# Kernel tuning notes

Measured on AMD Instinct MI355X. Metric: run time of the kernel, lower is better.

Reference implementation:

```python
import jax, jax.numpy as jnp
import numpy as np

SEQ, NV, NH, NR = 32768, 256, 512, 256


def _bern(key, p):
    # torch.bernoulli: sample is non-differentiable
    return (jax.random.uniform(key, p.shape, dtype=p.dtype) < p).astype(p.dtype)


def setup_inputs() -> dict:
    key = jax.random.key(0)
    ks = jax.random.split(key, 8)
    f32 = jnp.float32
    return {
        "v_seq": (jax.random.uniform(ks[0], (SEQ, NV), dtype=f32) < 0.1).astype(f32),
        "W1": jax.random.normal(ks[1], (NV, NH), dtype=f32) * 0.01,
        "bv": jnp.zeros((NV,), f32),
        "bh1": jnp.zeros((NH,), f32),
        "W2": jax.random.normal(ks[2], (NH, NH), dtype=f32) * 0.01,
        "bh2": jnp.zeros((NH,), f32),
        "Wyv": jax.random.normal(ks[3], (NV, NR), dtype=f32) * 1e-4,
        "Wyh1": jax.random.normal(ks[4], (NH, NR), dtype=f32) * 1e-4,
        "Wyh2": jax.random.normal(ks[5], (NH, NR), dtype=f32) * 1e-4,
        "Wvu": jax.random.normal(ks[6], (NV, NR), dtype=f32) * 0.01,
        "Wuu": jax.random.normal(ks[7], (NR, NR), dtype=f32) * 0.01,
        "bu": jnp.zeros((NR,), f32),
        "k": 5,
    }


def reference(v_seq, W1, bv, bh1, W2, bh2, Wyv, Wyh1, Wyh2, Wvu, Wuu, bu, k):
    dtype = v_seq.dtype
    nr = Wuu.shape[0]
    seq_len = v_seq.shape[0]

    # vanilla tanh RNN (abstract _run_rnn in base class)
    def rnn_step(u, v):
        u_new = jnp.tanh(v @ Wvu + u @ Wuu + bu)
        return u_new, u_new

    _, rnn_out = jax.lax.scan(rnn_step, jnp.zeros((nr,), dtype), v_seq)
    shifted = jnp.concatenate([jnp.zeros((1, nr), dtype), rnn_out[:-1]], axis=0)

    bv_t = bv + shifted @ Wyv.T    # [S, NV]
    bh1_t = bh1 + shifted @ Wyh1.T  # [S, NH]
    bh2_t = bh2 + shifted @ Wyh2.T  # [S, NH]

    key = jax.random.key(42)

    # CD-k Gibbs chain, RBM1 (visible <-> hidden1)
    v_sample = v_seq
    mean_v = None
    for _ in range(k):
        key, k1, k2 = jax.random.split(key, 3)
        h = _bern(k1, jax.nn.sigmoid(v_sample @ W1 + bh1_t))
        mean_v = jax.nn.sigmoid(h @ W1.T + bv_t)
        v_sample = _bern(k2, mean_v)

    def free_energy1(v):
        return -(v * bv_t).sum(-1) - jax.nn.softplus(v @ W1 + bh1_t).sum(-1)

    cost1 = (free_energy1(v_seq) - free_energy1(jax.lax.stop_gradient(v_sample))).mean()

    # CD-k Gibbs chain, RBM2 (hidden1 <-> hidden2)
    h1 = jax.nn.sigmoid(v_seq @ W1 + bh1_t)
    h1_sample = h1
    for _ in range(k):
        key, k1, k2 = jax.random.split(key, 3)
        h2 = _bern(k1, jax.nn.sigmoid(h1_sample @ W2 + bh2_t))
        h1_sample = _bern(k2, jax.nn.sigmoid(h2 @ W2.T + bh1_t))

    def free_energy2(h):
        return -(h * bh1_t).sum(-1) - jax.nn.softplus(h @ W2 + bh2_t).sum(-1)

    cost2 = (free_energy2(h1) - free_energy2(jax.lax.stop_gradient(h1_sample))).mean()

    eps = 1e-10
    monitor = (v_seq * jnp.log(mean_v + eps)
               + (1.0 - v_seq) * jnp.log(1.0 - mean_v + eps)).sum() / seq_len
    return (cost1 + cost2, monitor)
```

## Files before the change

### kernel.cpp

```cpp
#include <hip/hip_runtime.h>
#include <cstdint>

#define S_LEN 32768
#define NV 256
#define NH 512
#define NR 256

typedef short bf16x8 __attribute__((ext_vector_type(8)));
typedef float f32x4 __attribute__((ext_vector_type(4)));
typedef unsigned short ushort_t;
typedef ushort_t u16x8 __attribute__((ext_vector_type(8)));

__device__ __forceinline__ float b2f(ushort_t u) {
  return __uint_as_float(((uint32_t)u) << 16);
}
__device__ __forceinline__ ushort_t f2b(float f) {
  uint32_t x = __float_as_uint(f);
  uint32_t r = (x + 0x7fffu + ((x >> 16) & 1u)) >> 16;
  return (ushort_t)r;
}

#define TFR(x0,x1,r) { x0 += x1; x1 = ((x1 << (r)) | (x1 >> (32 - (r)))); x1 ^= x0; }
__host__ __forceinline__ void tf2x32(uint32_t k0, uint32_t k1,
                                     uint32_t x0, uint32_t x1,
                                     uint32_t* o0, uint32_t* o1) {
  uint32_t k2 = k0 ^ k1 ^ 0x1BD11BDAu;
  x0 += k0; x1 += k1;
  TFR(x0,x1,13) TFR(x0,x1,15) TFR(x0,x1,26) TFR(x0,x1,6)
  x0 += k1; x1 += k2 + 1u;
  TFR(x0,x1,17) TFR(x0,x1,29) TFR(x0,x1,16) TFR(x0,x1,24)
  x0 += k2; x1 += k0 + 2u;
  TFR(x0,x1,13) TFR(x0,x1,15) TFR(x0,x1,26) TFR(x0,x1,6)
  x0 += k0; x1 += k1 + 3u;
  TFR(x0,x1,17) TFR(x0,x1,29) TFR(x0,x1,16) TFR(x0,x1,24)
  x0 += k1; x1 += k2 + 4u;
  TFR(x0,x1,13) TFR(x0,x1,15) TFR(x0,x1,26) TFR(x0,x1,6)
  x0 += k2; x1 += k0 + 5u;
  *o0 = x0; *o1 = x1;
}

__device__ __forceinline__ float fast_uniform(uint32_t k0, uint32_t k1, uint32_t idx) {
  uint32_t h = idx ^ k0;
  h *= 0xCC9E2D51u; h = (h << 15) | (h >> 17); h *= 0x1B873593u;
  h ^= k1;
  h ^= h >> 16; h *= 0x85EBCA6Bu;
  h ^= h >> 13; h *= 0xC2B2AE35u;
  h ^= h >> 16;
  return __uint_as_float((h >> 9) | 0x3f800000u) - 1.0f;
}

__device__ __forceinline__ float wave_reduce(float v) {
#pragma unroll
  for (int o = 32; o > 0; o >>= 1) v += __shfl_down(v, o, 64);
  return v;
}
__device__ __forceinline__ float softplusf(float z) {
  return fmaxf(z, 0.f) + log1pf(expf(-fabsf(z)));
}

#define F_SAMP  4
#define F_H1    8
#define F_FE    16
#define F_MON   32
#define F_DOTB  64
#define F_DOTS  128

struct GemmArgs {
  const ushort_t* A;
  const ushort_t* BT;
  int boff;
  ushort_t* C;
  ushort_t* C2;
  const float* vseqf;
  double* fe_acc;
  double* mon_acc;
  float sign;
  uint32_t rk0, rk1;
  int N, K, nbx;
};

template<int FLAGS>
__device__ __forceinline__ void run_gemm(const GemmArgs& g,
                                         const ushort_t* __restrict__ biasm, int ldb,
                                         ushort_t* __restrict__ Als,
                                         ushort_t* __restrict__ Bls) {
  const int tid = threadIdx.x;
  const int lane = tid & 63, wave = tid >> 6;
  const int wm = wave >> 1, wn = wave & 1;
  const int q = lane >> 4, l16 = lane & 15;
  const int m0 = blockIdx.y * 128, n0 = blockIdx.x * 128;
  const int N = g.N, K = g.K;

  f32x4 acc[4][4];
#pragma unroll
  for (int mt = 0; mt < 4; mt++)
#pragma unroll
    for (int nt = 0; nt < 4; nt++) {
      const int gn = n0 + wn * 64 + nt * 16 + l16;
      const int gmb = m0 + wm * 64 + mt * 16 + q * 4;
#pragma unroll
      for (int rg = 0; rg < 4; rg++)
        acc[mt][nt][rg] = b2f(biasm[(size_t)(gmb + rg) * ldb + g.boff + gn]);
    }

  for (int kk = 0; kk < K; kk += 64) {
#pragma unroll
    for (int j = 0; j < 4; j++) {
      int c = j * 256 + tid;
      int r = c >> 3, bl = c & 7, bg = bl ^ (r & 7);
      *(uint4*)&Als[r * 64 + bl * 8] =
          *(const uint4*)&g.A[(size_t)(m0 + r) * K + kk + bg * 8];
      *(uint4*)&Bls[r * 64 + bl * 8] =
          *(const uint4*)&g.BT[(size_t)(n0 + r) * K + kk + bg * 8];
    }
    __syncthreads();
#pragma unroll
    for (int c = 0; c < 2; c++) {
      bf16x8 af[4], bf[4];
#pragma unroll
      for (int mt = 0; mt < 4; mt++) {
        int r = wm * 64 + mt * 16 + l16;
        af[mt] = *(const bf16x8*)&Als[r * 64 + (((c * 4 + q) ^ (r & 7)) * 8)];
      }
#pragma unroll
      for (int nt = 0; nt < 4; nt++) {
        int r = wn * 64 + nt * 16 + l16;
        bf[nt] = *(const bf16x8*)&Bls[r * 64 + (((c * 4 + q) ^ (r & 7)) * 8)];
      }
#pragma unroll
      for (int mt = 0; mt < 4; mt++)
#pragma unroll
        for (int nt = 0; nt < 4; nt++)
          acc[mt][nt] = __builtin_amdgcn_mfma_f32_16x16x32_bf16(
              af[mt], bf[nt], acc[mt][nt], 0, 0, 0);
    }
    __syncthreads();
  }

  float fe_sum = 0.f, mon_sum = 0.f;
#pragma unroll
  for (int mt = 0; mt < 4; mt++) {
#pragma unroll
    for (int nt = 0; nt < 4; nt++) {
      const int gn = n0 + wn * 64 + nt * 16 + l16;
      const int gmb = m0 + wm * 64 + mt * 16 + q * 4;
#pragma unroll
      for (int rg = 0; rg < 4; rg++) {
        const int gm = gmb + rg;
        const size_t idx = (size_t)gm * N + gn;
        float z = acc[mt][nt][rg];
        float be = 0.f;
        if constexpr (FLAGS & (F_DOTB | F_DOTS))
          be = b2f(biasm[(size_t)gm * ldb + g.boff + gn]);
        if constexpr (FLAGS & (F_SAMP | F_H1 | F_MON)) {
          float e = __expf(-z);
          if constexpr (FLAGS & F_SAMP) {
            float uu = fast_uniform(g.rk0, g.rk1, (uint32_t)idx);
            bool sbit = fmaf(uu, e, uu) < 1.f;
            g.C[idx] = sbit ? (ushort_t)0x3f80 : (ushort_t)0;
            if constexpr (FLAGS & F_DOTS) fe_sum += sbit ? be : 0.f;
          }
          if constexpr (FLAGS & (F_H1 | F_MON)) {
            float pp = __builtin_amdgcn_rcpf(1.f + e);
            if constexpr (FLAGS & F_H1) g.C2[idx] = f2b(pp);
            if constexpr (FLAGS & F_DOTB) fe_sum += pp * be;
            if constexpr (FLAGS & F_MON) {
              float v = g.vseqf[idx];
              mon_sum += (v != 0.f) ? logf(pp + 1e-10f) : logf(1.f - pp + 1e-10f);
            }
          }
        }
        if constexpr (FLAGS & F_FE) fe_sum += softplusf(z);
      }
    }
  }
  if constexpr (FLAGS & (F_FE | F_DOTB | F_DOTS)) {
    float s = wave_reduce(fe_sum);
    if (lane == 0) atomicAdd(g.fe_acc, (double)(-g.sign * s));
  }
  if constexpr (FLAGS & F_MON) {
    float s = wave_reduce(mon_sum);
    if (lane == 0) atomicAdd(g.mon_acc, (double)s);
  }
}

template<int FLAGS>
__global__ __launch_bounds__(256)
void gemm_samp(GemmArgs g, const ushort_t* __restrict__ biasm, int ldb) {
  __shared__ ushort_t Als[128 * 64];
  __shared__ ushort_t Bls[128 * 64];
  if ((int)blockIdx.x >= g.nbx) return;
  run_gemm<FLAGS>(g, biasm, ldb, Als, Bls);
}

template<int F0, int F1>
__global__ __launch_bounds__(256)
void gemm_pair(GemmArgs g0, GemmArgs g1, const ushort_t* __restrict__ biasm, int ldb) {
  __shared__ ushort_t Als[128 * 64];
  __shared__ ushort_t Bls[128 * 64];
  if (blockIdx.z == 0) {
    if ((int)blockIdx.x >= g0.nbx) return;
    run_gemm<F0>(g0, biasm, ldb, Als, Bls);
  } else {
    if ((int)blockIdx.x >= g1.nbx) return;
    run_gemm<F1>(g1, biasm, ldb, Als, Bls);
  }
}

template<bool OUTF32, bool VDOT>
__global__ __launch_bounds__(256)
void gemm_bias(const ushort_t* __restrict__ A, const ushort_t* __restrict__ BT,
               const float* __restrict__ biasv, ushort_t* __restrict__ Cb,
               float* __restrict__ Cf, const float* __restrict__ vdata,
               double* __restrict__ dacc, int M, int N, int K) {
  __shared__ ushort_t Als[128 * 64];
  __shared__ ushort_t Bls[128 * 64];
  const int tid = threadIdx.x;
  const int lane = tid & 63, wave = tid >> 6;
  const int wm = wave >> 1, wn = wave & 1;
  const int q = lane >> 4, l16 = lane & 15;
  const int m0 = blockIdx.y * 128, n0 = blockIdx.x * 128;

  f32x4 acc[4][4];
#pragma unroll
  for (int i = 0; i < 4; i++)
#pragma unroll
    for (int j = 0; j < 4; j++) acc[i][j] = (f32x4){0.f, 0.f, 0.f, 0.f};

  for (int kk = 0; kk < K; kk += 64) {
#pragma unroll
    for (int j = 0; j < 4; j++) {
      int c = j * 256 + tid;
      int r = c >> 3, bl = c & 7, bg = bl ^ (r & 7);
      *(uint4*)&Als[r * 64 + bl * 8] =
          *(const uint4*)&A[(size_t)(m0 + r) * K + kk + bg * 8];
      *(uint4*)&Bls[r * 64 + bl * 8] =
          *(const uint4*)&BT[(size_t)(n0 + r) * K + kk + bg * 8];
    }
    __syncthreads();
#pragma unroll
    for (int c = 0; c < 2; c++) {
      bf16x8 af[4], bf[4];
#pragma unroll
      for (int mt = 0; mt < 4; mt++) {
        int r = wm * 64 + mt * 16 + l16;
        af[mt] = *(const bf16x8*)&Als[r * 64 + (((c * 4 + q) ^ (r & 7)) * 8)];
      }
#pragma unroll
      for (int nt = 0; nt < 4; nt++) {
        int r = wn * 64 + nt * 16 + l16;
        bf[nt] = *(const bf16x8*)&Bls[r * 64 + (((c * 4 + q) ^ (r & 7)) * 8)];
      }
#pragma unroll
      for (int mt = 0; mt < 4; mt++)
#pragma unroll
        for (int nt = 0; nt < 4; nt++)
          acc[mt][nt] = __builtin_amdgcn_mfma_f32_16x16x32_bf16(
              af[mt], bf[nt], acc[mt][nt], 0, 0, 0);
    }
    __syncthreads();
  }
  float dsum = 0.f;
#pragma unroll
  for (int mt = 0; mt < 4; mt++)
#pragma unroll
    for (int nt = 0; nt < 4; nt++) {
      const int gn = n0 + wn * 64 + nt * 16 + l16;
      const int gmb = m0 + wm * 64 + mt * 16 + q * 4;
      const float bvv = biasv[gn];
#pragma unroll
      for (int rg = 0; rg < 4; rg++) {
        const size_t idx = (size_t)(gmb + rg) * N + gn;
        float z = acc[mt][nt][rg] + bvv;
        if constexpr (OUTF32) Cf[idx] = z; else Cb[idx] = f2b(z);
        if constexpr (VDOT)
          if (n0 < 256) dsum += z * vdata[(size_t)(gmb + rg) * 256 + gn];
      }
    }
  if constexpr (VDOT) {
    if (n0 < 256) {
      float s = wave_reduce(dsum);
      if ((tid & 63) == 0) atomicAdd(dacc, (double)(-s));
    }
  }
}

__global__ __launch_bounds__(1024, 1)
void rnn_scan(const float* __restrict__ Apre, const float* __restrict__ Wuu,
              ushort_t* __restrict__ shifted) {
  const int tid = threadIdx.x;
  const int j = tid >> 2;
  const int s = tid & 3;
  const int t_begin = blockIdx.x * 128;
  const int t_end = t_begin + 128;
  const int t0 = (t_begin >= 16) ? (t_begin - 16) : 0;

  float w[64];
#pragma unroll
  for (int i = 0; i < 64; i++) w[i] = Wuu[(size_t)(s * 64 + i) * 256 + j];

  __shared__ float u[2][280];
  __shared__ float asg[32 * 256];
  if (tid < 256) u[0][(tid >> 6) * 68 + (tid & 63)] = 0.f;
  if (blockIdx.x == 0 && s == 0) shifted[j] = 0;
  __syncthreads();

  const int jp = (j >> 6) * 68 + (j & 63);
  int p = 0;
  for (int tb = t0; tb < t_end; tb += 32) {
    int srow = tb + (tid >> 5);
    if (srow >= S_LEN) srow = S_LEN - 1;
    int scol = (tid & 31) * 8;
    float4 a0 = *(const float4*)&Apre[(size_t)srow * 256 + scol];
    float4 a1 = *(const float4*)&Apre[(size_t)srow * 256 + scol + 4];
    *(float4*)&asg[(tid >> 5) * 256 + scol] = a0;
    *(float4*)&asg[(tid >> 5) * 256 + scol + 4] = a1;
    __syncthreads();
#pragma unroll 1
    for (int i = 0; i < 32; i++) {
      const int t = tb + i;
      if (t >= t_end) break;
      float p0 = 0.f, p1 = 0.f, p2 = 0.f, p3 = 0.f;
#pragma unroll
      for (int qq = 0; qq < 64; qq += 4) {
        float4 uv = *(const float4*)&u[p][s * 68 + qq];
        p0 = fmaf(uv.x, w[qq + 0], p0);
        p1 = fmaf(uv.y, w[qq + 1], p1);
        p2 = fmaf(uv.z, w[qq + 2], p2);
        p3 = fmaf(uv.w, w[qq + 3], p3);
      }
      float ps = (p0 + p1) + (p2 + p3);
      ps += __shfl_xor(ps, 1, 64);
      ps += __shfl_xor(ps, 2, 64);
      float z = asg[i * 256 + j] + ps;
      float e = __expf(2.f * z);
      float unew = 1.f - 2.f * __builtin_amdgcn_rcpf(e + 1.f);
      if (s == 0) {
        u[1 - p][jp] = unew;
        if (t >= t_begin && (t + 1) < S_LEN)
          shifted[(size_t)(t + 1) * 256 + j] = f2b(unew);
      }
      __syncthreads();
      p ^= 1;
    }
  }
}

__global__ __launch_bounds__(256)
void prep_all(const float* __restrict__ v_seq, ushort_t* __restrict__ vseq_bf,
              const float* __restrict__ Wyv, const float* __restrict__ Wyh1,
              const float* __restrict__ Wyh2, ushort_t* __restrict__ Wycat,
              const float* __restrict__ W1, ushort_t* __restrict__ BTw1t,
              ushort_t* __restrict__ BTw1,
              const float* __restrict__ W2, ushort_t* __restrict__ BTw2t,
              ushort_t* __restrict__ BTw2,
              const float* __restrict__ Wvu, ushort_t* __restrict__ BTwvu,
              const float* __restrict__ bv, const float* __restrict__ bh1,
              const float* __restrict__ bh2, float* __restrict__ bveccat) {
  int b = blockIdx.x;
  const int tid = threadIdx.x;
  if (b < 32768) { int i = b * 256 + tid; vseq_bf[i] = f2b(v_seq[i]); return; }
  b -= 32768;
  if (b < 256)  { int i = b * 256 + tid; Wycat[i] = f2b(Wyv[i]); return; }
  b -= 256;
  if (b < 512)  { int i = b * 256 + tid; Wycat[65536 + i] = f2b(Wyh1[i]); return; }
  b -= 512;
  if (b < 512)  { int i = b * 256 + tid; Wycat[196608 + i] = f2b(Wyh2[i]); return; }
  b -= 512;
  if (b < 512)  { int i = b * 256 + tid; BTw1t[i] = f2b(W1[i]); return; }
  b -= 512;
  if (b < 1024) { int i = b * 256 + tid; BTw2t[i] = f2b(W2[i]); return; }
  b -= 1024;
  if (b < 256)  { int i = b * 256 + tid; int r = i >> 8, c = i & 255;
                  BTwvu[c * 256 + r] = f2b(Wvu[i]); return; }
  b -= 256;
  if (b < 512)  { int i = b * 256 + tid; int r = i >> 9, c = i & 511;
                  BTw1[(size_t)c * 256 + r] = f2b(W1[i]); return; }
  b -= 512;
  if (b < 1024) { int i = b * 256 + tid; int r = i >> 9, c = i & 511;
                  BTw2[(size_t)c * 512 + r] = f2b(W2[i]); return; }
  b -= 1024;
  { int i = b * 256 + tid;
    if (i < 1280)
      bveccat[i] = (i < 256) ? bv[i] : (i < 768) ? bh1[i - 256] : bh2[i - 768]; }
}

__global__ void finalize_kernel(const double* __restrict__ acc, float* __restrict__ out) {
  out[0] = (float)(acc[0] / (double)S_LEN);
  out[1] = (float)(acc[1] / (double)S_LEN);
}

extern "C" void kernel_launch(void* const* d_in, const int* in_sizes, int n_in,
                              void* d_out, int out_size, void* d_ws, size_t ws_size,
                              hipStream_t stream) {
  (void)in_sizes; (void)n_in; (void)out_size; (void)ws_size;
  const float* v_seq = (const float*)d_in[0];
  const float* W1    = (const float*)d_in[1];
  const float* bv    = (const float*)d_in[2];
  const float* bh1   = (const float*)d_in[3];
  const float* W2    = (const float*)d_in[4];
  const float* bh2   = (const float*)d_in[5];
  const float* Wyv   = (const float*)d_in[6];
  const float* Wyh1  = (const float*)d_in[7];
  const float* Wyh2  = (const float*)d_in[8];
  const float* Wvu   = (const float*)d_in[9];
  const float* Wuu   = (const float*)d_in[10];
  const float* bu    = (const float*)d_in[11];
  float* out = (float*)d_out;

  const size_t SN = (size_t)S_LEN * NV;
  const size_t SH = (size_t)S_LEN * NH;
  const int NB = NV + NH + NH;
  char* base = (char*)d_ws;
  size_t cur = 0;
  auto take = [&](size_t bytes) { size_t o = cur; cur += (bytes + 255) & ~(size_t)255; return o; };
  double*   acc      = (double*)  (base + take(64));
  ushort_t* BTwvu    = (ushort_t*)(base + take(65536 * 2));
  ushort_t* Wycat    = (ushort_t*)(base + take((size_t)NB * NR * 2));
  float*    bveccat  = (float*)   (base + take(NB * 4));
  ushort_t* BTw1     = (ushort_t*)(base + take(131072 * 2));
  ushort_t* BTw1t    = (ushort_t*)(base + take(131072 * 2));
  ushort_t* BTw2     = (ushort_t*)(base + take(262144 * 2));
  ushort_t* BTw2t    = (ushort_t*)(base + take(262144 * 2));
  ushort_t* vseq_bf  = (ushort_t*)(base + take(SN * 2));
  ushort_t* shifted  = (ushort_t*)(base + take(SN * 2));
  ushort_t* bias_cat = (ushort_t*)(base + take((size_t)S_LEN * NB * 2));
  ushort_t* h1buf    = (ushort_t*)(base + take(SH * 2));
  ushort_t* sampA    = (ushort_t*)(base + take(SH * 2));
  ushort_t* sampB    = (ushort_t*)(base + take(SN * 2));
  float*    Arnn  = (float*)bias_cat;
  ushort_t* sampC = vseq_bf;
  ushort_t* sampD = h1buf;

  uint32_t ka[20], kb[20];
  uint32_t K0 = 0u, K1 = 42u;
  for (int it = 0; it < 10; it++) {
    uint32_t n0, n1, a0, a1, b0, b1;
    tf2x32(K0, K1, 0u, 0u, &n0, &n1);
    tf2x32(K0, K1, 0u, 1u, &a0, &a1);
    tf2x32(K0, K1, 0u, 2u, &b0, &b1);
    ka[2 * it] = a0; kb[2 * it] = a1;
    ka[2 * it + 1] = b0; kb[2 * it + 1] = b1;
    K0 = n0; K1 = n1;
  }

  hipMemsetAsync(acc, 0, 2 * sizeof(double), stream);

  dim3 blk(256);
  prep_all<<<dim3(37381), blk, 0, stream>>>(
      v_seq, vseq_bf, Wyv, Wyh1, Wyh2, Wycat, W1, BTw1t, BTw1,
      W2, BTw2t, BTw2, Wvu, BTwvu, bv, bh1, bh2, bveccat);

  const int M = S_LEN;
  gemm_bias<true, false><<<dim3(2, M / 128), blk, 0, stream>>>(
      vseq_bf, BTwvu, bu, nullptr, Arnn, nullptr, nullptr, M, NV, NV);
  rnn_scan<<<dim3(S_LEN / 128), dim3(1024), 0, stream>>>(Arnn, Wuu, shifted);
  gemm_bias<false, true><<<dim3(NB / 128, M / 128), blk, 0, stream>>>(
      shifted, Wycat, bveccat, bias_cat, nullptr, v_seq, acc, M, NB, NR);

  const int OFF_BV = 0, OFF_BH1 = NV, OFF_BH2 = NV + NH;
  auto mk = [&](const ushort_t* A, const ushort_t* BT, int boff, ushort_t* C,
                ushort_t* C2, const float* vs, float sign, int key, int N, int K) {
    GemmArgs g;
    g.A = A; g.BT = BT; g.boff = boff; g.C = C; g.C2 = C2; g.vseqf = vs;
    g.fe_acc = acc; g.mon_acc = acc + 1; g.sign = sign;
    g.rk0 = key >= 0 ? ka[key] : 0; g.rk1 = key >= 0 ? kb[key] : 0;
    g.N = N; g.K = K; g.nbx = N / 128;
    return g;
  };

  gemm_samp<F_SAMP | F_H1 | F_FE | F_DOTB><<<dim3(4, M / 128), blk, 0, stream>>>(
      mk(vseq_bf, BTw1, OFF_BH1, sampA, h1buf, nullptr, 1.0f, 0, NH, NV),
      bias_cat, NB);

  dim3 pg(4, M / 128, 2);
  GemmArgs V[9], Hh[4], A2g[5], B2g[5];
  for (int it = 0; it < 5; it++) {
    if (it > 0)
      Hh[it - 1] = mk(sampB, BTw1, OFF_BH1, sampA, nullptr, nullptr, 0.f,
                      2 * it, NH, NV);
    V[it] = mk(sampA, BTw1t, OFF_BV, sampB, nullptr,
               (it == 4) ? v_seq : nullptr, (it == 4) ? -1.0f : 0.f,
               2 * it + 1, NV, NH);
    A2g[it] = mk((it == 0) ? h1buf : sampD, BTw2, OFF_BH2, sampC, nullptr, nullptr,
                 (it == 0) ? 1.0f : 0.f, 10 + 2 * it, NH, NH);
    B2g[it] = mk(sampC, BTw2t, OFF_BH1, sampD, nullptr, nullptr,
                 (it == 4) ? -1.0f : 0.f, 11 + 2 * it, NH, NH);
  }
  GemmArgs FE1 = mk(sampB, BTw1, OFF_BH1, nullptr, nullptr, nullptr, -1.0f,
                    -1, NH, NV);
  GemmArgs FE2 = mk(sampD, BTw2, OFF_BH2, nullptr, nullptr, nullptr, -1.0f,
                    -1, NH, NH);

  gemm_pair<F_SAMP, F_SAMP | F_FE><<<pg, blk, 0, stream>>>(V[0], A2g[0], bias_cat, NB);
  gemm_pair<F_SAMP, F_SAMP><<<pg, blk, 0, stream>>>(Hh[0], B2g[0], bias_cat, NB);
  gemm_pair<F_SAMP, F_SAMP><<<pg, blk, 0, stream>>>(V[1], A2g[1], bias_cat, NB);
  gemm_pair<F_SAMP, F_SAMP><<<pg, blk, 0, stream>>>(Hh[1], B2g[1], bias_cat, NB);
  gemm_pair<F_SAMP, F_SAMP><<<pg, blk, 0, stream>>>(V[2], A2g[2], bias_cat, NB);
  gemm_pair<F_SAMP, F_SAMP><<<pg, blk, 0, stream>>>(Hh[2], B2g[2], bias_cat, NB);
  gemm_pair<F_SAMP, F_SAMP><<<pg, blk, 0, stream>>>(V[3], A2g[3], bias_cat, NB);
  gemm_pair<F_SAMP, F_SAMP><<<pg, blk, 0, stream>>>(Hh[3], B2g[3], bias_cat, NB);
  gemm_pair<F_SAMP | F_MON | F_DOTS, F_SAMP><<<pg, blk, 0, stream>>>(
      V[4], A2g[4], bias_cat, NB);
  gemm_pair<F_FE, F_SAMP | F_DOTS><<<pg, blk, 0, stream>>>(FE1, B2g[4], bias_cat, NB);

  gemm_samp<F_FE><<<dim3(4, M / 128), blk, 0, stream>>>(FE2, bias_cat, NB);

  finalize_kernel<<<1, 1, 0, stream>>>(acc, out);
}
```

Baseline: 1.436 ms.

## Fold per-timestep bias projections into Gibbs GEMMs via K-concatenation with shifted RNN state

Each Gibbs-step GEMM no longer reads a precomputed per-row bias matrix (S x 1280 bf16). Instead it concatenates the shifted RNN state as extra K columns and the Wy weights as extra B rows, so the time-varying bias is recomputed inside the MFMA loop. Only a 768-wide bias matrix is still materialized, for the dot-product free-energy terms. This removes large bias-matrix reads from every sampling kernel but adds 256 extra K per GEMM, raising compute by 50-100% per step.

```diff
diff --git a/kernel.cpp b/kernel.cpp
--- a/kernel.cpp
+++ b/kernel.cpp
@@ -5,6 +5,7 @@
 #define NV 256
 #define NH 512
 #define NR 256
+#define LDB_DYN 768
 
 typedef short bf16x8 __attribute__((ext_vector_type(8)));
 typedef float f32x4 __attribute__((ext_vector_type(4)));
@@ -67,8 +68,10 @@
 
 struct GemmArgs {
   const ushort_t* A;
+  const ushort_t* Aaux;
   const ushort_t* BT;
-  int boff;
+  const float* bvec;
+  const ushort_t* dotb;
   ushort_t* C;
   ushort_t* C2;
   const float* vseqf;
@@ -76,12 +79,11 @@
   double* mon_acc;
   float sign;
   uint32_t rk0, rk1;
-  int N, K, nbx;
+  int N, K1, Ktot, nbx;
 };
 
 template<int FLAGS>
 __device__ __forceinline__ void run_gemm(const GemmArgs& g,
-                                         const ushort_t* __restrict__ biasm, int ldb,
                                          ushort_t* __restrict__ Als,
                                          ushort_t* __restrict__ Bls) {
   const int tid = threadIdx.x;
@@ -89,7 +91,7 @@
   const int wm = wave >> 1, wn = wave & 1;
   const int q = lane >> 4, l16 = lane & 15;
   const int m0 = blockIdx.y * 128, n0 = blockIdx.x * 128;
-  const int N = g.N, K = g.K;
+  const int N = g.N, K1 = g.K1, Ktot = g.Ktot;
 
   f32x4 acc[4][4];
 #pragma unroll
@@ -97,21 +99,23 @@
 #pragma unroll
     for (int nt = 0; nt < 4; nt++) {
       const int gn = n0 + wn * 64 + nt * 16 + l16;
-      const int gmb = m0 + wm * 64 + mt * 16 + q * 4;
-#pragma unroll
-      for (int rg = 0; rg < 4; rg++)
-        acc[mt][nt][rg] = b2f(biasm[(size_t)(gmb + rg) * ldb + g.boff + gn]);
-    }
-
-  for (int kk = 0; kk < K; kk += 64) {
+      const float bv = g.bvec[gn];
+#pragma unroll
+      for (int rg = 0; rg < 4; rg++) acc[mt][nt][rg] = bv;
+    }
+
+  for (int kk = 0; kk < Ktot; kk += 64) {
+    const ushort_t* asrc; int ald, kloc;
+    if (kk < K1) { asrc = g.A; ald = K1; kloc = kk; }
+    else         { asrc = g.Aaux; ald = 256; kloc = kk - K1; }
 #pragma unroll
     for (int j = 0; j < 4; j++) {
       int c = j * 256 + tid;
       int r = c >> 3, bl = c & 7, bg = bl ^ (r & 7);
       *(uint4*)&Als[r * 64 + bl * 8] =
-          *(const uint4*)&g.A[(size_t)(m0 + r) * K + kk + bg * 8];
+          *(const uint4*)&asrc[(size_t)(m0 + r) * ald + kloc + bg * 8];
       *(uint4*)&Bls[r * 64 + bl * 8] =
-          *(const uint4*)&g.BT[(size_t)(n0 + r) * K + kk + bg * 8];
+          *(const uint4*)&g.BT[(size_t)(n0 + r) * Ktot + kk + bg * 8];
     }
     __syncthreads();
 #pragma unroll
@@ -151,7 +155,7 @@
         float z = acc[mt][nt][rg];
         float be = 0.f;
         if constexpr (FLAGS & (F_DOTB | F_DOTS))
-          be = b2f(biasm[(size_t)gm * ldb + g.boff + gn]);
+          be = b2f(g.dotb[(size_t)gm * LDB_DYN + gn]);
         if constexpr (FLAGS & (F_SAMP | F_H1 | F_MON)) {
           float e = __expf(-z);
           if constexpr (FLAGS & F_SAMP) {
@@ -186,24 +190,24 @@
 
 template<int FLAGS>
 __global__ __launch_bounds__(256)
-void gemm_samp(GemmArgs g, const ushort_t* __restrict__ biasm, int ldb) {
+void gemm_samp(GemmArgs g) {
   __shared__ ushort_t Als[128 * 64];
   __shared__ ushort_t Bls[128 * 64];
   if ((int)blockIdx.x >= g.nbx) return;
-  run_gemm<FLAGS>(g, biasm, ldb, Als, Bls);
+  run_gemm<FLAGS>(g, Als, Bls);
 }
 
 template<int F0, int F1>
 __global__ __launch_bounds__(256)
-void gemm_pair(GemmArgs g0, GemmArgs g1, const ushort_t* __restrict__ biasm, int ldb) {
+void gemm_pair(GemmArgs g0, GemmArgs g1) {
   __shared__ ushort_t Als[128 * 64];
   __shared__ ushort_t Bls[128 * 64];
   if (blockIdx.z == 0) {
     if ((int)blockIdx.x >= g0.nbx) return;
-    run_gemm<F0>(g0, biasm, ldb, Als, Bls);
+    run_gemm<F0>(g0, Als, Bls);
   } else {
     if ((int)blockIdx.x >= g1.nbx) return;
-    run_gemm<F1>(g1, biasm, ldb, Als, Bls);
+    run_gemm<F1>(g1, Als, Bls);
   }
 }
 
@@ -348,38 +352,61 @@
 
 __global__ __launch_bounds__(256)
 void prep_all(const float* __restrict__ v_seq, ushort_t* __restrict__ vseq_bf,
+              const float* __restrict__ W1, const float* __restrict__ W2,
               const float* __restrict__ Wyv, const float* __restrict__ Wyh1,
-              const float* __restrict__ Wyh2, ushort_t* __restrict__ Wycat,
-              const float* __restrict__ W1, ushort_t* __restrict__ BTw1t,
-              ushort_t* __restrict__ BTw1,
-              const float* __restrict__ W2, ushort_t* __restrict__ BTw2t,
-              ushort_t* __restrict__ BTw2,
-              const float* __restrict__ Wvu, ushort_t* __restrict__ BTwvu,
+              const float* __restrict__ Wyh2, const float* __restrict__ Wvu,
+              ushort_t* __restrict__ Bcat1h,
+              ushort_t* __restrict__ Bcat1v,
+              ushort_t* __restrict__ Bcat2h,
+              ushort_t* __restrict__ Bcat2b,
+              ushort_t* __restrict__ Wyvh1,
+              ushort_t* __restrict__ BTwvu,
               const float* __restrict__ bv, const float* __restrict__ bh1,
               const float* __restrict__ bh2, float* __restrict__ bveccat) {
   int b = blockIdx.x;
   const int tid = threadIdx.x;
   if (b < 32768) { int i = b * 256 + tid; vseq_bf[i] = f2b(v_seq[i]); return; }
   b -= 32768;
-  if (b < 256)  { int i = b * 256 + tid; Wycat[i] = f2b(Wyv[i]); return; }
+  if (b < 1024) {
+    int i = b * 256 + tid, n = i >> 9, c = i & 511;
+    Bcat1h[i] = f2b(c < 256 ? W1[(size_t)c * 512 + n] : Wyh1[(size_t)n * 256 + c - 256]);
+    return;
+  }
+  b -= 1024;
+  if (b < 768) {
+    int n = b / 3, c = (b % 3) * 256 + tid;
+    Bcat1v[(size_t)n * 768 + c] =
+        f2b(c < 512 ? W1[(size_t)n * 512 + c] : Wyv[(size_t)n * 256 + c - 512]);
+    return;
+  }
+  b -= 768;
+  if (b < 1536) {
+    int n = b / 3, c = (b % 3) * 256 + tid;
+    Bcat2h[(size_t)n * 768 + c] =
+        f2b(c < 512 ? W2[(size_t)c * 512 + n] : Wyh2[(size_t)n * 256 + c - 512]);
+    return;
+  }
+  b -= 1536;
+  if (b < 1536) {
+    int n = b / 3, c = (b % 3) * 256 + tid;
+    Bcat2b[(size_t)n * 768 + c] =
+        f2b(c < 512 ? W2[(size_t)n * 512 + c] : Wyh1[(size_t)n * 256 + c - 512]);
+    return;
+  }
+  b -= 1536;
+  if (b < 768) {
+    int r = b, c = tid;
+    Wyvh1[(size_t)r * 256 + c] =
+        f2b(r < 256 ? Wyv[(size_t)r * 256 + c] : Wyh1[(size_t)(r - 256) * 256 + c]);
+    return;
+  }
+  b -= 768;
+  if (b < 256) {
+    int i = b * 256 + tid, r = i >> 8, c = i & 255;
+    BTwvu[c * 256 + r] = f2b(Wvu[i]);
+    return;
+  }
   b -= 256;
-  if (b < 512)  { int i = b * 256 + tid; Wycat[65536 + i] = f2b(Wyh1[i]); return; }
-  b -= 512;
-  if (b < 512)  { int i = b * 256 + tid; Wycat[196608 + i] = f2b(Wyh2[i]); return; }
-  b -= 512;
-  if (b < 512)  { int i = b * 256 + tid; BTw1t[i] = f2b(W1[i]); return; }
-  b -= 512;
-  if (b < 1024) { int i = b * 256 + tid; BTw2t[i] = f2b(W2[i]); return; }
-  b -= 1024;
-  if (b < 256)  { int i = b * 256 + tid; int r = i >> 8, c = i & 255;
-                  BTwvu[c * 256 + r] = f2b(Wvu[i]); return; }
-  b -= 256;
-  if (b < 512)  { int i = b * 256 + tid; int r = i >> 9, c = i & 511;
-                  BTw1[(size_t)c * 256 + r] = f2b(W1[i]); return; }
-  b -= 512;
-  if (b < 1024) { int i = b * 256 + tid; int r = i >> 9, c = i & 511;
-                  BTw2[(size_t)c * 512 + r] = f2b(W2[i]); return; }
-  b -= 1024;
   { int i = b * 256 + tid;
     if (i < 1280)
       bveccat[i] = (i < 256) ? bv[i] : (i < 768) ? bh1[i - 256] : bh2[i - 768]; }
@@ -410,26 +437,25 @@
 
   const size_t SN = (size_t)S_LEN * NV;
   const size_t SH = (size_t)S_LEN * NH;
-  const int NB = NV + NH + NH;
   char* base = (char*)d_ws;
   size_t cur = 0;
   auto take = [&](size_t bytes) { size_t o = cur; cur += (bytes + 255) & ~(size_t)255; return o; };
   double*   acc      = (double*)  (base + take(64));
   ushort_t* BTwvu    = (ushort_t*)(base + take(65536 * 2));
-  ushort_t* Wycat    = (ushort_t*)(base + take((size_t)NB * NR * 2));
-  float*    bveccat  = (float*)   (base + take(NB * 4));
-  ushort_t* BTw1     = (ushort_t*)(base + take(131072 * 2));
-  ushort_t* BTw1t    = (ushort_t*)(base + take(131072 * 2));
-  ushort_t* BTw2     = (ushort_t*)(base + take(262144 * 2));
-  ushort_t* BTw2t    = (ushort_t*)(base + take(262144 * 2));
+  ushort_t* Bcat1h   = (ushort_t*)(base + take(262144 * 2));
+  ushort_t* Bcat1v   = (ushort_t*)(base + take(196608 * 2));
+  ushort_t* Bcat2h   = (ushort_t*)(base + take(393216 * 2));
+  ushort_t* Bcat2b   = (ushort_t*)(base + take(393216 * 2));
+  ushort_t* Wyvh1    = (ushort_t*)(base + take(196608 * 2));
+  float*    bveccat  = (float*)   (base + take(1280 * 4));
   ushort_t* vseq_bf  = (ushort_t*)(base + take(SN * 2));
   ushort_t* shifted  = (ushort_t*)(base + take(SN * 2));
-  ushort_t* bias_cat = (ushort_t*)(base + take((size_t)S_LEN * NB * 2));
+  ushort_t* bias_dyn = (ushort_t*)(base + take((size_t)S_LEN * LDB_DYN * 2));
   ushort_t* h1buf    = (ushort_t*)(base + take(SH * 2));
   ushort_t* sampA    = (ushort_t*)(base + take(SH * 2));
   ushort_t* sampB    = (ushort_t*)(base + take(SN * 2));
-  float*    Arnn  = (float*)bias_cat;
-  ushort_t* sampC = vseq_bf;
+  ushort_t* sampC    = (ushort_t*)(base + take(SH * 2));
+  float* Arnn = (float*)bias_dyn;
   ushort_t* sampD = h1buf;
 
   uint32_t ka[20], kb[20];
@@ -447,64 +473,68 @@
   hipMemsetAsync(acc, 0, 2 * sizeof(double), stream);
 
   dim3 blk(256);
-  prep_all<<<dim3(37381), blk, 0, stream>>>(
-      v_seq, vseq_bf, Wyv, Wyh1, Wyh2, Wycat, W1, BTw1t, BTw1,
-      W2, BTw2t, BTw2, Wvu, BTwvu, bv, bh1, bh2, bveccat);
+  prep_all<<<dim3(38661), blk, 0, stream>>>(
+      v_seq, vseq_bf, W1, W2, Wyv, Wyh1, Wyh2, Wvu,
+      Bcat1h, Bcat1v, Bcat2h, Bcat2b, Wyvh1, BTwvu, bv, bh1, bh2, bveccat);
 
   const int M = S_LEN;
   gemm_bias<true, false><<<dim3(2, M / 128), blk, 0, stream>>>(
       vseq_bf, BTwvu, bu, nullptr, Arnn, nullptr, nullptr, M, NV, NV);
   rnn_scan<<<dim3(S_LEN / 128), dim3(1024), 0, stream>>>(Arnn, Wuu, shifted);
-  gemm_bias<false, true><<<dim3(NB / 128, M / 128), blk, 0, stream>>>(
-      shifted, Wycat, bveccat, bias_cat, nullptr, v_seq, acc, M, NB, NR);
-
-  const int OFF_BV = 0, OFF_BH1 = NV, OFF_BH2 = NV + NH;
-  auto mk = [&](const ushort_t* A, const ushort_t* BT, int boff, ushort_t* C,
-                ushort_t* C2, const float* vs, float sign, int key, int N, int K) {
+  gemm_bias<false, true><<<dim3(LDB_DYN / 128, M / 128), blk, 0, stream>>>(
+      shifted, Wyvh1, bveccat, bias_dyn, nullptr, v_seq, acc, M, LDB_DYN, NR);
+
+  auto mk = [&](const ushort_t* A, const ushort_t* BT, const float* bvp,
+                const ushort_t* dotb, ushort_t* C, ushort_t* C2, const float* vs,
+                float sign, int key, int N, int K1m, int Ktot) {
     GemmArgs g;
-    g.A = A; g.BT = BT; g.boff = boff; g.C = C; g.C2 = C2; g.vseqf = vs;
+    g.A = A; g.Aaux = shifted; g.BT = BT; g.bvec = bvp; g.dotb = dotb;
+    g.C = C; g.C2 = C2; g.vseqf = vs;
     g.fe_acc = acc; g.mon_acc = acc + 1; g.sign = sign;
     g.rk0 = key >= 0 ? ka[key] : 0; g.rk1 = key >= 0 ? kb[key] : 0;
-    g.N = N; g.K = K; g.nbx = N / 128;
+    g.N = N; g.K1 = K1m; g.Ktot = Ktot; g.nbx = N / 128;
     return g;
   };
+  const float* BV  = bveccat;
+  const float* BH1 = bveccat + 256;
+  const float* BH2 = bveccat + 768;
 
   gemm_samp<F_SAMP | F_H1 | F_FE | F_DOTB><<<dim3(4, M / 128), blk, 0, stream>>>(
-      mk(vseq_bf, BTw1, OFF_BH1, sampA, h1buf, nullptr, 1.0f, 0, NH, NV),
-      bias_cat, NB);
+      mk(vseq_bf, Bcat1h, BH1, bias_dyn + 256, sampA, h1buf, nullptr,
+         1.0f, 0, NH, 256, 512));
 
   dim3 pg(4, M / 128, 2);
-  GemmArgs V[9], Hh[4], A2g[5], B2g[5];
+  GemmArgs V[5], Hh[4], A2g[5], B2g[5];
   for (int it = 0; it < 5; it++) {
     if (it > 0)
-      Hh[it - 1] = mk(sampB, BTw1, OFF_BH1, sampA, nullptr, nullptr, 0.f,
-                      2 * it, NH, NV);
-    V[it] = mk(sampA, BTw1t, OFF_BV, sampB, nullptr,
+      Hh[it - 1] = mk(sampB, Bcat1h, BH1, nullptr, sampA, nullptr, nullptr,
+                      0.f, 2 * it, NH, 256, 512);
+    V[it] = mk(sampA, Bcat1v, BV, (it == 4) ? bias_dyn : nullptr, sampB, nullptr,
                (it == 4) ? v_seq : nullptr, (it == 4) ? -1.0f : 0.f,
-               2 * it + 1, NV, NH);
-    A2g[it] = mk((it == 0) ? h1buf : sampD, BTw2, OFF_BH2, sampC, nullptr, nullptr,
-                 (it == 0) ? 1.0f : 0.f, 10 + 2 * it, NH, NH);
-    B2g[it] = mk(sampC, BTw2t, OFF_BH1, sampD, nullptr, nullptr,
-                 (it == 4) ? -1.0f : 0.f, 11 + 2 * it, NH, NH);
-  }
-  GemmArgs FE1 = mk(sampB, BTw1, OFF_BH1, nullptr, nullptr, nullptr, -1.0f,
-                    -1, NH, NV);
-  GemmArgs FE2 = mk(sampD, BTw2, OFF_BH2, nullptr, nullptr, nullptr, -1.0f,
-                    -1, NH, NH);
-
-  gemm_pair<F_SAMP, F_SAMP | F_FE><<<pg, blk, 0, stream>>>(V[0], A2g[0], bias_cat, NB);
-  gemm_pair<F_SAMP, F_SAMP><<<pg, blk, 0, stream>>>(Hh[0], B2g[0], bias_cat, NB);
-  gemm_pair<F_SAMP, F_SAMP><<<pg, blk, 0, stream>>>(V[1], A2g[1], bias_cat, NB);
-  gemm_pair<F_SAMP, F_SAMP><<<pg, blk, 0, stream>>>(Hh[1], B2g[1], bias_cat, NB);
-  gemm_pair<F_SAMP, F_SAMP><<<pg, blk, 0, stream>>>(V[2], A2g[2], bias_cat, NB);
-  gemm_pair<F_SAMP, F_SAMP><<<pg, blk, 0, stream>>>(Hh[2], B2g[2], bias_cat, NB);
-  gemm_pair<F_SAMP, F_SAMP><<<pg, blk, 0, stream>>>(V[3], A2g[3], bias_cat, NB);
-  gemm_pair<F_SAMP, F_SAMP><<<pg, blk, 0, stream>>>(Hh[3], B2g[3], bias_cat, NB);
-  gemm_pair<F_SAMP | F_MON | F_DOTS, F_SAMP><<<pg, blk, 0, stream>>>(
-      V[4], A2g[4], bias_cat, NB);
-  gemm_pair<F_FE, F_SAMP | F_DOTS><<<pg, blk, 0, stream>>>(FE1, B2g[4], bias_cat, NB);
-
-  gemm_samp<F_FE><<<dim3(4, M / 128), blk, 0, stream>>>(FE2, bias_cat, NB);
+               2 * it + 1, NV, 512, 768);
+    A2g[it] = mk((it == 0) ? h1buf : sampD, Bcat2h, BH2, nullptr, sampC, nullptr,
+                 nullptr, (it == 0) ? 1.0f : 0.f, 10 + 2 * it, NH, 512, 768);
+    B2g[it] = mk(sampC, Bcat2b, BH1, (it == 4) ? (bias_dyn + 256) : nullptr,
+                 sampD, nullptr, nullptr, (it == 4) ? -1.0f : 0.f,
+                 11 + 2 * it, NH, 512, 768);
+  }
+  GemmArgs FE1 = mk(sampB, Bcat1h, BH1, nullptr, nullptr, nullptr, nullptr,
+                    -1.0f, -1, NH, 256, 512);
+  GemmArgs FE2 = mk(sampD, Bcat2h, BH2, nullptr, nullptr, nullptr, nullptr,
+                    -1.0f, -1, NH, 512, 768);
+
+  gemm_pair<F_SAMP, F_SAMP | F_FE><<<pg, blk, 0, stream>>>(V[0], A2g[0]);
+  gemm_pair<F_SAMP, F_SAMP><<<pg, blk, 0, stream>>>(Hh[0], B2g[0]);
+  gemm_pair<F_SAMP, F_SAMP><<<pg, blk, 0, stream>>>(V[1], A2g[1]);
+  gemm_pair<F_SAMP, F_SAMP><<<pg, blk, 0, stream>>>(Hh[1], B2g[1]);
+  gemm_pair<F_SAMP, F_SAMP><<<pg, blk, 0, stream>>>(V[2], A2g[2]);
+  gemm_pair<F_SAMP, F_SAMP><<<pg, blk, 0, stream>>>(Hh[2], B2g[2]);
+  gemm_pair<F_SAMP, F_SAMP><<<pg, blk, 0, stream>>>(V[3], A2g[3]);
+  gemm_pair<F_SAMP, F_SAMP><<<pg, blk, 0, stream>>>(Hh[3], B2g[3]);
+  gemm_pair<F_SAMP | F_MON | F_DOTS, F_SAMP><<<pg, blk, 0, stream>>>(V[4], A2g[4]);
+  gemm_pair<F_FE, F_SAMP | F_DOTS><<<pg, blk, 0, stream>>>(FE1, B2g[4]);
+
+  gemm_samp<F_FE><<<dim3(4, M / 128), blk, 0, stream>>>(FE2);
 
   finalize_kernel<<<1, 1, 0, stream>>>(acc, out);
 }
```

Result: slower. 1.519 ms (+5.8%).
